# Kernel optimization log

Measured on AMD Instinct MI355X. Metric: run time of the kernel, lower is better.

The kernel has to match this reference:

```python
import jax, jax.numpy as jnp
import numpy as np

HEADS = 8
SPLITS = 4


def setup_inputs() -> dict:
    key = jax.random.key(0)
    ks = jax.random.split(key, 5)
    B, C, N = 8, 512, 4096
    C2 = C // 2
    x = jax.random.normal(ks[0], (B, C, N), jnp.float32)
    # reduction: Conv1d(C -> C//2, k=1) => weight [C2, C], bias [C2]
    Wr = jax.random.normal(ks[1], (C2, C), jnp.float32) * (1.0 / np.sqrt(C))
    br = jnp.zeros((C2,), jnp.float32)
    # toQKV: Linear(C2 -> 3*C2, bias=False); stored as [in, out]
    Wqkv = jax.random.normal(ks[2], (C2, 3 * C2), jnp.float32) * (1.0 / np.sqrt(C2))
    # expansion: Conv1d(C2 -> C, k=1) => weight [C, C2], bias [C]
    We = jax.random.normal(ks[3], (C, C2), jnp.float32) * (1.0 / np.sqrt(C2))
    be = jnp.zeros((C,), jnp.float32)
    return {"x": x, "Wr": Wr, "br": br, "Wqkv": Wqkv, "We": We, "be": be}


def reference(x, Wr, br, Wqkv, We, be):
    B, C, N = x.shape
    h, S = HEADS, SPLITS
    # 1x1 conv reduction: [B, C, N] -> [B, C2, N]
    y = jnp.einsum('oc,bcn->bon', Wr, x) + br[None, :, None]
    t = y.transpose(0, 2, 1)                       # [B, N, C2]
    qkv = t @ Wqkv                                 # [B, N, 3*C2]
    q, k, v = jnp.split(qkv, 3, axis=-1)
    d = q.shape[-1] // h
    n = N // S

    def to_chunks(a):
        # b n (h d) -> b h S n' d  (block-diagonal chunks along the token dim)
        return a.reshape(B, N, h, d).transpose(0, 2, 1, 3).reshape(B, h, S, n, d)

    q, k, v = to_chunks(q), to_chunks(k), to_chunks(v)
    scale = d ** -0.5
    scores = jnp.einsum('bhsnd,bhsmd->bhsnm', q, k) * scale   # [B,h,S,n,n]
    attn = jax.nn.softmax(scores, axis=-1)
    o = jnp.einsum('bhsnm,bhsmd->bhsnd', attn, v)             # [B,h,S,n,d]
    # rearrange per-chunk to 'b n (h d)' and concat chunks along n (restores order)
    o = o.transpose(0, 2, 3, 1, 4).reshape(B, N, h * d)       # [B, N, C2]
    o = o.transpose(0, 2, 1)                                  # [B, C2, N]
    out = jnp.einsum('oc,bcn->bon', We, o) + be[None, :, None]  # [B, C, N]
    return out
```

## Files before the change

kernel.cpp:

```cpp
#include <hip/hip_runtime.h>
#include <hip/hip_bf16.h>

#define BATCH 8
#define CIN   512
#define NTOK  4096
#define CH    256
#define J3    768
#define NH    8
#define DH    32
#define NCH   1024

typedef _Float16 F16;
typedef _Float16 f16x8 __attribute__((ext_vector_type(8)));
typedef _Float16 f16x4 __attribute__((ext_vector_type(4)));
typedef _Float16 f16x2 __attribute__((ext_vector_type(2)));
typedef float    f32x4  __attribute__((ext_vector_type(4)));
typedef float    f32x16 __attribute__((ext_vector_type(16)));

#define QSCALE 0.25503483f


__global__ __launch_bounds__(256) void fuse_weights_kernel(
    const float* __restrict__ Wr, const float* __restrict__ br,
    const float* __restrict__ Wqkv,
    F16* __restrict__ Wc_t, float* __restrict__ bcomb)
{
    const int j0 = blockIdx.x * 2;
    const int tid = threadIdx.x;
    float a00 = 0.f, a01 = 0.f, a10 = 0.f, a11 = 0.f;
    for (int c2 = 0; c2 < CH; ++c2) {
        const float w0 = Wr[c2 * CIN + tid];
        const float w1 = Wr[c2 * CIN + tid + 256];
        const float q0 = Wqkv[c2 * J3 + j0];
        const float q1 = Wqkv[c2 * J3 + j0 + 1];
        a00 = fmaf(w0, q0, a00);
        a01 = fmaf(w1, q0, a01);
        a10 = fmaf(w0, q1, a10);
        a11 = fmaf(w1, q1, a11);
    }
    const int c0 = tid, c1 = tid + 256;
    const int off0 = (c0 >> 5) * 8192 + ((c0 >> 3) & 3) * 2048 + (c0 & 7);
    const int off1 = (c1 >> 5) * 8192 + ((c1 >> 3) & 3) * 2048 + (c1 & 7);
#pragma unroll
    for (int jj = 0; jj < 2; ++jj) {
        const int j = j0 + jj;
        const float qs = (j < 256) ? QSCALE : 1.0f;
        const int jb = j >> 8, row = j & 255;
        const float v0 = jj ? a10 : a00, v1 = jj ? a11 : a01;
        Wc_t[jb * 131072 + off0 + row * 8] = (F16)(v0 * qs);
        Wc_t[jb * 131072 + off1 + row * 8] = (F16)(v1 * qs);
    }
    if (tid < 2) {
        const int j = j0 + tid;
        const float qs = (j < 256) ? QSCALE : 1.0f;
        float s = 0.f;
        for (int c2 = 0; c2 < CH; ++c2) s = fmaf(Wqkv[c2 * J3 + j], br[c2], s);
        bcomb[j] = s * qs;
    }
}

__global__ __launch_bounds__(256) void convert_we_kernel(
    const float* __restrict__ We, F16* __restrict__ We_t)
{
    const int i = blockIdx.x * 256 + threadIdx.x;
    const int j = i >> 8, c2 = i & 255;
    We_t[(j >> 7) * 32768 + (c2 >> 5) * 4096 + ((c2 >> 3) & 3) * 1024 +
         (j & 127) * 8 + (c2 & 7)] = (F16)We[i];
}

__global__ __launch_bounds__(256) void transpose_convert_kernel(
    const float* __restrict__ x, F16* __restrict__ xt_t)
{
    const int b = blockIdx.z;
    const int c0 = blockIdx.y * 8;
    const int n = blockIdx.x * 256 + threadIdx.x;

    const float* xb = x + ((size_t)b * CIN + c0) * NTOK + n;
    f16x8 v;
#pragma unroll
    for (int i = 0; i < 8; ++i)
        v[i] = (F16)xb[(size_t)i * NTOK];

    const int nb = n >> 7, row = n & 127;
    const int t = c0 >> 5, kg = (c0 >> 3) & 3;
    *(f16x8*)&xt_t[(size_t)b * 2097152 + nb * 65536 + t * 4096 + kg * 1024 +
                   row * 8] = v;
}

__global__ __launch_bounds__(512, 4) void gemm1_kernel(
    const F16* __restrict__ A,
    const F16* __restrict__ B,
    const float* __restrict__ bias,
    F16* __restrict__ Qb,
    F16* __restrict__ Kt,
    F16* __restrict__ Vt)
{
    const int b  = blockIdx.z;
    const int jb = blockIdx.y;
    const int j0 = jb * 256;
    const int nb = blockIdx.x;
    const int n0 = nb * 128;
    const int tid = threadIdx.x;
    const int w = tid >> 6, l = tid & 63;
    const int wr = w >> 1;
    const int wc = w & 1;
    const int cl = l & 15, rg = l >> 4;

    __shared__ __align__(16) char smem[49152];
    F16* Ash0 = (F16*)smem;
    F16* Ash1 = (F16*)(smem + 16384);
    F16* Bsh0 = (F16*)(smem + 32768);
    F16* Bsh1 = (F16*)(smem + 40960);
    F16* Esh  = (F16*)smem;

    f32x4 acc[4][4];
#pragma unroll
    for (int i = 0; i < 4; ++i)
#pragma unroll
        for (int j = 0; j < 4; ++j) acc[i][j] = (f32x4){0.f, 0.f, 0.f, 0.f};

    const F16* Abase = A + jb * 131072 + tid * 8;
    const F16* Bbase = B + (size_t)b * 2097152 + nb * 65536 + tid * 8;

#define G1_STAGE(Adst, Bdst, t)                                                \
    do {                                                                       \
        __builtin_amdgcn_global_load_lds(                                      \
            (const __attribute__((address_space(1))) void*)(Abase + (t) * 8192),\
            (__attribute__((address_space(3))) void*)&Adst[tid * 8], 16, 0, 0);\
        __builtin_amdgcn_global_load_lds(                                      \
            (const __attribute__((address_space(1))) void*)(Abase + (t) * 8192 \
                + 4096),                                                       \
            (__attribute__((address_space(3))) void*)&Adst[4096 + tid * 8],    \
            16, 0, 0);                                                         \
        __builtin_amdgcn_global_load_lds(                                      \
            (const __attribute__((address_space(1))) void*)(Bbase + (t) * 4096),\
            (__attribute__((address_space(3))) void*)&Bdst[tid * 8], 16, 0, 0);\
    } while (0)

    G1_STAGE(Ash0, Bsh0, 0);
    __syncthreads();

    for (int t = 0; t < 16; ++t) {
        F16* Ac = (t & 1) ? Ash1 : Ash0;
        F16* Bc = (t & 1) ? Bsh1 : Bsh0;
        if (t < 15) {
            F16* An = (t & 1) ? Ash0 : Ash1;
            F16* Bn = (t & 1) ? Bsh0 : Bsh1;
            G1_STAGE(An, Bn, t + 1);
        }
        f16x8 bf[4];
#pragma unroll
        for (int j = 0; j < 4; ++j)
            bf[j] = *(const f16x8*)&Bc[rg * 1024 + (wc * 64 + j * 16 + cl) * 8];
#pragma unroll
        for (int i = 0; i < 4; ++i) {
            const f16x8 af =
                *(const f16x8*)&Ac[rg * 2048 + (wr * 64 + i * 16 + cl) * 8];
#pragma unroll
            for (int j = 0; j < 4; ++j)
                acc[i][j] = __builtin_amdgcn_mfma_f32_16x16x32_f16(
                    af, bf[j], acc[i][j], 0, 0, 0);
        }
        __syncthreads();
    }
#undef G1_STAGE

    const int sidx = n0 >> 10;
    const int tb   = (n0 >> 6) & 15;

    if (jb < 2) {
        const size_t bN = (size_t)b * NTOK;
#pragma unroll
        for (int c = 0; c < 4; ++c) {
            if (c) __syncthreads();
            if (wc == (c >> 1)) {
#pragma unroll
                for (int i = 0; i < 4; ++i) {
#pragma unroll
                    for (int jj = 0; jj < 2; ++jj) {
                        const int jn = (c & 1) * 2 + jj;
                        const int nl = jj * 16 + cl;
                        const int jl = wr * 64 + i * 16 + rg * 4;
                        const int jg = j0 + jl;
                        f16x4 v;
#pragma unroll
                        for (int r = 0; r < 4; ++r)
                            v[r] = (F16)(acc[i][jn][r] + bias[jg + r]);
                        *(f16x4*)&Esh[nl * 264 + jl] = v;
                    }
                }
            }
            __syncthreads();
            if (jb == 0) {
                const int rr = tid >> 4, ss = tid & 15;
                const f16x8 ov0 = *(const f16x8*)&Esh[rr * 264 + ss * 16];
                const f16x8 ov1 = *(const f16x8*)&Esh[rr * 264 + ss * 16 + 8];
                F16* dst = &Qb[(bN + n0 + c * 32 + rr) * 256 + ss * 16];
                *(f16x8*)dst = ov0;
                *(f16x8*)(dst + 8) = ov1;
            } else {
                const int tloc = (tb + (c >> 1)) & 15;
#pragma unroll
                for (int p = 0; p < 2; ++p) {
                    const int uid = tid + p * 512;
                    const int nl = uid & 31, kg = (uid >> 5) & 3,
                              hh = uid >> 7;
                    const f16x8 ov =
                        *(const f16x8*)&Esh[nl * 264 + hh * 32 + kg * 8];
                    const int nk = (c & 1) * 32 + nl;
                    *(f16x8*)&Kt[(((size_t)b * NH + hh) * 4 + sidx) * 32768 +
                                 tloc * 2048 + kg * 512 + nk * 8] = ov;
                }
            }
        }
    } else {
#pragma unroll
        for (int c = 0; c < 4; ++c) {
            if (c) __syncthreads();
            if (wr == c) {
#pragma unroll
                for (int i = 0; i < 4; ++i) {
                    const int jg = j0 + c * 64 + i * 16 + rg * 4;
#pragma unroll
                    for (int jn = 0; jn < 4; ++jn) {
                        const int nl = wc * 64 + jn * 16 + cl;
#pragma unroll
                        for (int r = 0; r < 4; ++r)
                            Esh[(i * 16 + rg * 4 + r) * 136 + nl] =
                                (F16)(acc[i][jn][r] + bias[jg + r]);
                    }
                }
            }
            __syncthreads();
#pragma unroll
            for (int p = 0; p < 2; ++p) {
                const int uid = tid + p * 512;
                const int d = uid & 31, vg = (uid >> 5) & 7,
                          ttv = (uid >> 8) & 1, hl = uid >> 9;
                const int hh = c * 2 + hl;
                const int tloc = (tb + ttv) & 15;
                const f16x8 ov =
                    *(const f16x8*)&Esh[(hl * 32 + d) * 136 + ttv * 64 + vg * 8];
                *(f16x8*)&Vt[(((size_t)b * NH + hh) * 4 + sidx) * 32768 +
                             tloc * 2048 + vg * 256 + d * 8] = ov;
            }
        }
    }
}

__global__ __launch_bounds__(256, 4) void attn_mfma_kernel(
    const F16* __restrict__ Qb,
    const F16* __restrict__ Kt,
    const F16* __restrict__ Vt,
    F16* __restrict__ O)
{
    const int bid = blockIdx.x;
    const int xcd = bid & 7, tt = bid >> 3;
    const int qpair = tt & 3;
    const int pr = xcd * 32 + (tt >> 2);
    const int s = pr & 3, bh = pr >> 2;
    const int b = bh >> 3, h = bh & 7;
    const int tid = threadIdx.x;
    const int w = tid >> 6, l = tid & 63;
    const int ln = l & 31;
    const int hi = l >> 5;

    __shared__ __align__(16) F16 Klds[2][64 * 40];
    __shared__ __align__(16) F16 Vlds[2][32 * 68];

    const size_t bN = (size_t)b * NTOK + (size_t)s * NCH;
    const int q0 = qpair * 256 + w * 64;

    const F16* Qpa = Qb + (bN + q0 + ln) * 256 + h * DH + hi * 8;
    const F16* Qpb = Qpa + 32 * 256;
    const f16x8 qfa0 = *(const f16x8*)Qpa;
    const f16x8 qfa1 = *(const f16x8*)(Qpa + 16);
    const f16x8 qfb0 = *(const f16x8*)Qpb;
    const f16x8 qfb1 = *(const f16x8*)(Qpb + 16);

    const F16* Kbase = Kt + (((size_t)b * NH + h) * 4 + s) * 32768 + tid * 8;
    const F16* Vbase = Vt + (((size_t)b * NH + h) * 4 + s) * 32768 + tid * 8;
    const int kw = (tid & 63) * 40 + (tid >> 6) * 8;
    const int vw = (tid & 31) * 68 + (tid >> 5) * 8;

    f16x8 kreg = *(const f16x8*)Kbase;
    f16x8 vreg = *(const f16x8*)Vbase;

    f32x16 oacca = (f32x16)(0.0f);
    f32x16 oaccb = (f32x16)(0.0f);
    float lsum_a = 0.f, lsum_b = 0.f;

    *(f16x8*)&Klds[0][kw] = kreg;
    *(f16x4*)&Vlds[0][vw] = __builtin_shufflevector(vreg, vreg, 0, 1, 2, 3);
    *(f16x4*)&Vlds[0][vw + 4] = __builtin_shufflevector(vreg, vreg, 4, 5, 6, 7);

    for (int t = 0; t < 16; ++t) {
        const int cur = t & 1, nxt = cur ^ 1;
        __syncthreads();
        if (t < 15) {
            kreg = *(const f16x8*)(Kbase + (t + 1) * 2048);
            vreg = *(const f16x8*)(Vbase + (t + 1) * 2048);
        }
        const F16* Kb = &Klds[cur][0];
        const F16* Vb = &Vlds[cur][0];
#pragma unroll
        for (int u = 0; u < 2; ++u) {
            const int nkb = u * 32;
            const f16x8 kf0 = *(const f16x8*)&Kb[(nkb + ln) * 40 + hi * 8];
            const f16x8 kf1 = *(const f16x8*)&Kb[(nkb + ln) * 40 + 16 + hi * 8];

            f32x16 sacc = (f32x16)(0.0f);
            __builtin_amdgcn_s_setprio(1);
            sacc = __builtin_amdgcn_mfma_f32_32x32x16_f16(kf0, qfa0, sacc, 0, 0, 0);
            sacc = __builtin_amdgcn_mfma_f32_32x32x16_f16(kf1, qfa1, sacc, 0, 0, 0);
            __builtin_amdgcn_s_setprio(0);
            union { f16x8 v; f16x2 h[4]; } pa0, pa1, pb0, pb1;
#pragma unroll
            for (int e = 0; e < 4; ++e) {
                pa0.h[e] = __builtin_bit_cast(f16x2, __builtin_amdgcn_cvt_pkrtz(
                    __builtin_amdgcn_exp2f(sacc[2 * e]),
                    __builtin_amdgcn_exp2f(sacc[2 * e + 1])));
                pa1.h[e] = __builtin_bit_cast(f16x2, __builtin_amdgcn_cvt_pkrtz(
                    __builtin_amdgcn_exp2f(sacc[8 + 2 * e]),
                    __builtin_amdgcn_exp2f(sacc[8 + 2 * e + 1])));
            }
            {
                const f16x2 t01 = pa0.h[0] + pa0.h[1] + pa1.h[0] + pa1.h[1];
                const f16x2 t23 = pa0.h[2] + pa0.h[3] + pa1.h[2] + pa1.h[3];
                const f16x2 ts = t01 + t23;
                lsum_a += (float)ts[0] + (float)ts[1];
            }

            f32x16 sb = (f32x16)(0.0f);
            __builtin_amdgcn_s_setprio(1);
            sb = __builtin_amdgcn_mfma_f32_32x32x16_f16(kf0, qfb0, sb, 0, 0, 0);
            sb = __builtin_amdgcn_mfma_f32_32x32x16_f16(kf1, qfb1, sb, 0, 0, 0);
            __builtin_amdgcn_s_setprio(0);
#pragma unroll
            for (int e = 0; e < 4; ++e) {
                pb0.h[e] = __builtin_bit_cast(f16x2, __builtin_amdgcn_cvt_pkrtz(
                    __builtin_amdgcn_exp2f(sb[2 * e]),
                    __builtin_amdgcn_exp2f(sb[2 * e + 1])));
                pb1.h[e] = __builtin_bit_cast(f16x2, __builtin_amdgcn_cvt_pkrtz(
                    __builtin_amdgcn_exp2f(sb[8 + 2 * e]),
                    __builtin_amdgcn_exp2f(sb[8 + 2 * e + 1])));
            }
            {
                const f16x2 t01 = pb0.h[0] + pb0.h[1] + pb1.h[0] + pb1.h[1];
                const f16x2 t23 = pb0.h[2] + pb0.h[3] + pb1.h[2] + pb1.h[3];
                const f16x2 ts = t01 + t23;
                lsum_b += (float)ts[0] + (float)ts[1];
            }

            const int vbase = ln * 68 + nkb + 4 * hi;
            const f16x4 v00 = *(const f16x4*)&Vb[vbase];
            const f16x4 v01 = *(const f16x4*)&Vb[vbase + 8];
            const f16x4 v10 = *(const f16x4*)&Vb[vbase + 16];
            const f16x4 v11 = *(const f16x4*)&Vb[vbase + 24];
            const f16x8 vf0 = __builtin_shufflevector(v00, v01, 0, 1, 2, 3, 4, 5, 6, 7);
            const f16x8 vf1 = __builtin_shufflevector(v10, v11, 0, 1, 2, 3, 4, 5, 6, 7);

            __builtin_amdgcn_s_setprio(1);
            oacca = __builtin_amdgcn_mfma_f32_32x32x16_f16(pa0.v, vf0, oacca, 0, 0, 0);
            oacca = __builtin_amdgcn_mfma_f32_32x32x16_f16(pa1.v, vf1, oacca, 0, 0, 0);
            oaccb = __builtin_amdgcn_mfma_f32_32x32x16_f16(pb0.v, vf0, oaccb, 0, 0, 0);
            oaccb = __builtin_amdgcn_mfma_f32_32x32x16_f16(pb1.v, vf1, oaccb, 0, 0, 0);
            __builtin_amdgcn_s_setprio(0);
        }
        if (t < 15) {
            *(f16x8*)&Klds[nxt][kw] = kreg;
            *(f16x4*)&Vlds[nxt][vw] =
                __builtin_shufflevector(vreg, vreg, 0, 1, 2, 3);
            *(f16x4*)&Vlds[nxt][vw + 4] =
                __builtin_shufflevector(vreg, vreg, 4, 5, 6, 7);
        }
    }

    lsum_a += __shfl_xor(lsum_a, 32);
    lsum_b += __shfl_xor(lsum_b, 32);
    __syncthreads();
    float* Ltab = (float*)&Vlds[0][0] + w * 64;
    if (hi == 0) {
        Ltab[ln] = lsum_a;
        Ltab[32 + ln] = lsum_b;
    }
    F16* Elds = (F16*)&Klds[0][0] + w * 1152;
    const int q = ln;
#pragma unroll
    for (int set = 0; set < 2; ++set) {
        const f32x16 oacc = set ? oaccb : oacca;
#pragma unroll
        for (int r = 0; r < 16; ++r) {
            const int qr = (r & 3) + 8 * (r >> 2) + 4 * hi;
            const float invr = __builtin_amdgcn_rcpf(Ltab[set * 32 + qr]);
            Elds[qr * 36 + ln] = (F16)(oacc[r] * invr);
        }
        const int g = qpair * 256 + w * 64 + set * 32;
        const int nb = s * 8 + (g >> 7);
        const int row0 = g & 127;
        F16* Ob = O + (size_t)b * 1048576 + nb * 32768 + h * 4096;
#pragma unroll
        for (int st = 0; st < 2; ++st) {
            const int kg = hi + 2 * st;
            const f16x8 ov = *(const f16x8*)&Elds[q * 36 + kg * 8];
            *(f16x8*)&Ob[kg * 1024 + (row0 + q) * 8] = ov;
        }
    }
}

__global__ __launch_bounds__(256) void gemm2_kernel(
    const F16* __restrict__ A,
    const F16* __restrict__ B,
    const float* __restrict__ bias,
    float* __restrict__ Y)
{
    const int b  = blockIdx.z;
    const int jb = blockIdx.y;
    const int j0 = jb * 128;
    const int nb = blockIdx.x;
    const int n0 = nb * 128;
    const int tid = threadIdx.x;
    const int w = tid >> 6, l = tid & 63;
    const int wr = w >> 1, wc = w & 1;
    const int cl = l & 15, rg = l >> 4;

    __shared__ __align__(16) F16 Ash[2][4096];
    __shared__ __align__(16) F16 Bsh[2][4096];

    f32x4 acc[4][4];
#pragma unroll
    for (int i = 0; i < 4; ++i)
#pragma unroll
        for (int j = 0; j < 4; ++j) acc[i][j] = (f32x4){0.f, 0.f, 0.f, 0.f};

    const int frag_off = rg * 1024 + cl * 8;
    const F16* Abase = A + jb * 32768 + tid * 8;
    const F16* Bbase = B + (size_t)b * 1048576 + nb * 32768 + tid * 8;

#define G2_STAGE(bu, t)                                                        \
    do {                                                                       \
        __builtin_amdgcn_global_load_lds(                                      \
            (const __attribute__((address_space(1))) void*)(Abase + (t) * 4096),\
            (__attribute__((address_space(3))) void*)&Ash[bu][tid * 8],        \
            16, 0, 0);                                                         \
        __builtin_amdgcn_global_load_lds(                                      \
            (const __attribute__((address_space(1))) void*)(Abase + (t) * 4096 \
                + 2048),                                                       \
            (__attribute__((address_space(3))) void*)&Ash[bu][2048 + tid * 8], \
            16, 0, 0);                                                         \
        __builtin_amdgcn_global_load_lds(                                      \
            (const __attribute__((address_space(1))) void*)(Bbase + (t) * 4096),\
            (__attribute__((address_space(3))) void*)&Bsh[bu][tid * 8],        \
            16, 0, 0);                                                         \
        __builtin_amdgcn_global_load_lds(                                      \
            (const __attribute__((address_space(1))) void*)(Bbase + (t) * 4096 \
                + 2048),                                                       \
            (__attribute__((address_space(3))) void*)&Bsh[bu][2048 + tid * 8], \
            16, 0, 0);                                                         \
    } while (0)

    G2_STAGE(0, 0);
    __syncthreads();

    for (int t = 0; t < 8; ++t) {
        const int cur = t & 1;
        if (t < 7) G2_STAGE(cur ^ 1, t + 1);

        f16x8 af[4], bfr[4];
#pragma unroll
        for (int f = 0; f < 4; ++f) {
            af[f]  = *(const f16x8*)&Ash[cur][frag_off + (wr * 64 + f * 16) * 8];
            bfr[f] = *(const f16x8*)&Bsh[cur][frag_off + (wc * 64 + f * 16) * 8];
        }
#pragma unroll
        for (int i = 0; i < 4; ++i)
#pragma unroll
            for (int j = 0; j < 4; ++j)
                acc[i][j] = __builtin_amdgcn_mfma_f32_16x16x32_f16(
                    af[i], bfr[j], acc[i][j], 0, 0, 0);
        __syncthreads();
    }
#undef G2_STAGE

#pragma unroll
    for (int i = 0; i < 4; ++i) {
        const int jj = j0 + wr * 64 + i * 16 + rg * 4;
#pragma unroll
        for (int j = 0; j < 4; ++j) {
            const int nn = n0 + wc * 64 + j * 16 + cl;
#pragma unroll
            for (int r = 0; r < 4; ++r)
                Y[((size_t)b * CIN + jj + r) * NTOK + nn] =
                    acc[i][j][r] + bias[jj + r];
        }
    }
}

extern "C" void kernel_launch(void* const* d_in, const int* in_sizes, int n_in,
                              void* d_out, int out_size, void* d_ws, size_t ws_size,
                              hipStream_t stream)
{
    const float* x    = (const float*)d_in[0];
    const float* Wr   = (const float*)d_in[1];
    const float* br   = (const float*)d_in[2];
    const float* Wqkv = (const float*)d_in[3];
    const float* We   = (const float*)d_in[4];
    const float* be   = (const float*)d_in[5];
    float* out = (float*)d_out;

    char* ws = (char*)d_ws;
    F16*   Wc    = (F16*)ws;      ws += 786432;
    float* bcomb = (float*)ws;    ws += 4096;
    F16*   We_t  = (F16*)ws;      ws += 262144;
    F16*   Qb    = (F16*)ws;      ws += (size_t)BATCH * NTOK * 256 * 2;
    F16*   Kt    = (F16*)ws;      ws += (size_t)BATCH * NH * 4 * 32768 * 2;
    F16*   Vt    = (F16*)ws;      ws += (size_t)BATCH * NH * 4 * 32768 * 2;
    F16*   xt    = (F16*)ws;
    F16*   O_t   = (F16*)ws;

    fuse_weights_kernel<<<J3 / 2, 256, 0, stream>>>(Wr, br, Wqkv, Wc, bcomb);
    convert_we_kernel<<<CIN * CH / 256, 256, 0, stream>>>(We, We_t);
    transpose_convert_kernel<<<dim3(NTOK / 256, CIN / 8, BATCH), 256, 0, stream>>>(x, xt);
    gemm1_kernel<<<dim3(NTOK / 128, J3 / 256, BATCH), 512, 0, stream>>>(
        Wc, xt, bcomb, Qb, Kt, Vt);
    attn_mfma_kernel<<<1024, 256, 0, stream>>>(Qb, Kt, Vt, O_t);
    gemm2_kernel<<<dim3(NTOK / 128, CIN / 128, BATCH), 256, 0, stream>>>(
        We_t, O_t, be, out);
}
```

Measured before the change: 154.7 us.

## Load K/V fragments directly from global memory, drop LDS staging and barriers

Result: slower. 354.8 us (+129.4%).

```diff
diff --git a/kernel.cpp b/kernel.cpp
--- a/kernel.cpp
+++ b/kernel.cpp
@@ -248,7 +248,7 @@
     }
 }
 
-__global__ __launch_bounds__(256, 4) void attn_mfma_kernel(
+__global__ __launch_bounds__(256, 8) void attn_mfma_kernel(
     const F16* __restrict__ Qb,
     const F16* __restrict__ Kt,
     const F16* __restrict__ Vt,
@@ -265,8 +265,8 @@
     const int ln = l & 31;
     const int hi = l >> 5;
 
-    __shared__ __align__(16) F16 Klds[2][64 * 40];
-    __shared__ __align__(16) F16 Vlds[2][32 * 68];
+    __shared__ __align__(16) F16 Epi[4][1152];
+    __shared__ __align__(16) float Ltab_s[4][64];
 
     const size_t bN = (size_t)b * NTOK + (size_t)s * NCH;
     const int q0 = qpair * 256 + w * 64;
@@ -278,36 +278,20 @@
     const f16x8 qfb0 = *(const f16x8*)Qpb;
     const f16x8 qfb1 = *(const f16x8*)(Qpb + 16);
 
-    const F16* Kbase = Kt + (((size_t)b * NH + h) * 4 + s) * 32768 + tid * 8;
-    const F16* Vbase = Vt + (((size_t)b * NH + h) * 4 + s) * 32768 + tid * 8;
-    const int kw = (tid & 63) * 40 + (tid >> 6) * 8;
-    const int vw = (tid & 31) * 68 + (tid >> 5) * 8;
-
-    f16x8 kreg = *(const f16x8*)Kbase;
-    f16x8 vreg = *(const f16x8*)Vbase;
+    const F16* Kb = Kt + (((size_t)b * NH + h) * 4 + s) * 32768;
+    const F16* Vb = Vt + (((size_t)b * NH + h) * 4 + s) * 32768;
 
     f32x16 oacca = (f32x16)(0.0f);
     f32x16 oaccb = (f32x16)(0.0f);
     float lsum_a = 0.f, lsum_b = 0.f;
 
-    *(f16x8*)&Klds[0][kw] = kreg;
-    *(f16x4*)&Vlds[0][vw] = __builtin_shufflevector(vreg, vreg, 0, 1, 2, 3);
-    *(f16x4*)&Vlds[0][vw + 4] = __builtin_shufflevector(vreg, vreg, 4, 5, 6, 7);
-
     for (int t = 0; t < 16; ++t) {
-        const int cur = t & 1, nxt = cur ^ 1;
-        __syncthreads();
-        if (t < 15) {
-            kreg = *(const f16x8*)(Kbase + (t + 1) * 2048);
-            vreg = *(const f16x8*)(Vbase + (t + 1) * 2048);
-        }
-        const F16* Kb = &Klds[cur][0];
-        const F16* Vb = &Vlds[cur][0];
 #pragma unroll
         for (int u = 0; u < 2; ++u) {
-            const int nkb = u * 32;
-            const f16x8 kf0 = *(const f16x8*)&Kb[(nkb + ln) * 40 + hi * 8];
-            const f16x8 kf1 = *(const f16x8*)&Kb[(nkb + ln) * 40 + 16 + hi * 8];
+            const f16x8 kf0 =
+                *(const f16x8*)&Kb[t * 2048 + hi * 512 + (u * 32 + ln) * 8];
+            const f16x8 kf1 =
+                *(const f16x8*)&Kb[t * 2048 + (2 + hi) * 512 + (u * 32 + ln) * 8];
 
             f32x16 sacc = (f32x16)(0.0f);
             __builtin_amdgcn_s_setprio(1);
@@ -352,11 +336,11 @@
                 lsum_b += (float)ts[0] + (float)ts[1];
             }
 
-            const int vbase = ln * 68 + nkb + 4 * hi;
-            const f16x4 v00 = *(const f16x4*)&Vb[vbase];
-            const f16x4 v01 = *(const f16x4*)&Vb[vbase + 8];
-            const f16x4 v10 = *(const f16x4*)&Vb[vbase + 16];
-            const f16x4 v11 = *(const f16x4*)&Vb[vbase + 24];
+            const int vb0 = t * 2048 + (u * 4) * 256 + ln * 8 + 4 * hi;
+            const f16x4 v00 = *(const f16x4*)&Vb[vb0];
+            const f16x4 v01 = *(const f16x4*)&Vb[vb0 + 256];
+            const f16x4 v10 = *(const f16x4*)&Vb[vb0 + 512];
+            const f16x4 v11 = *(const f16x4*)&Vb[vb0 + 768];
             const f16x8 vf0 = __builtin_shufflevector(v00, v01, 0, 1, 2, 3, 4, 5, 6, 7);
             const f16x8 vf1 = __builtin_shufflevector(v10, v11, 0, 1, 2, 3, 4, 5, 6, 7);
 
@@ -367,24 +351,16 @@
             oaccb = __builtin_amdgcn_mfma_f32_32x32x16_f16(pb1.v, vf1, oaccb, 0, 0, 0);
             __builtin_amdgcn_s_setprio(0);
         }
-        if (t < 15) {
-            *(f16x8*)&Klds[nxt][kw] = kreg;
-            *(f16x4*)&Vlds[nxt][vw] =
-                __builtin_shufflevector(vreg, vreg, 0, 1, 2, 3);
-            *(f16x4*)&Vlds[nxt][vw + 4] =
-                __builtin_shufflevector(vreg, vreg, 4, 5, 6, 7);
-        }
     }
 
     lsum_a += __shfl_xor(lsum_a, 32);
     lsum_b += __shfl_xor(lsum_b, 32);
-    __syncthreads();
-    float* Ltab = (float*)&Vlds[0][0] + w * 64;
+    float* Ltab = &Ltab_s[w][0];
     if (hi == 0) {
         Ltab[ln] = lsum_a;
         Ltab[32 + ln] = lsum_b;
     }
-    F16* Elds = (F16*)&Klds[0][0] + w * 1152;
+    F16* Elds = &Epi[w][0];
     const int q = ln;
 #pragma unroll
     for (int set = 0; set < 2; ++set) {
```

## Enlarge gemm2 output tile to 256 rows with 512-thread blocks

Applied to the files above, without the earlier changes.

Result: no change. 153.6 us (-0.7%).

```diff
diff --git a/kernel.cpp b/kernel.cpp
--- a/kernel.cpp
+++ b/kernel.cpp
@@ -64,8 +64,8 @@
 {
     const int i = blockIdx.x * 256 + threadIdx.x;
     const int j = i >> 8, c2 = i & 255;
-    We_t[(j >> 7) * 32768 + (c2 >> 5) * 4096 + ((c2 >> 3) & 3) * 1024 +
-         (j & 127) * 8 + (c2 & 7)] = (F16)We[i];
+    We_t[(j >> 8) * 65536 + (c2 >> 5) * 8192 + ((c2 >> 3) & 3) * 2048 +
+         (j & 255) * 8 + (c2 & 7)] = (F16)We[i];
 }
 
 __global__ __launch_bounds__(256) void transpose_convert_kernel(
@@ -408,7 +408,7 @@
     }
 }
 
-__global__ __launch_bounds__(256) void gemm2_kernel(
+__global__ __launch_bounds__(512, 4) void gemm2_kernel(
     const F16* __restrict__ A,
     const F16* __restrict__ B,
     const float* __restrict__ bias,
@@ -416,16 +416,20 @@
 {
     const int b  = blockIdx.z;
     const int jb = blockIdx.y;
-    const int j0 = jb * 128;
+    const int j0 = jb * 256;
     const int nb = blockIdx.x;
     const int n0 = nb * 128;
     const int tid = threadIdx.x;
     const int w = tid >> 6, l = tid & 63;
-    const int wr = w >> 1, wc = w & 1;
+    const int wr = w >> 1;
+    const int wc = w & 1;
     const int cl = l & 15, rg = l >> 4;
 
-    __shared__ __align__(16) F16 Ash[2][4096];
-    __shared__ __align__(16) F16 Bsh[2][4096];
+    __shared__ __align__(16) char smem[49152];
+    F16* Ash0 = (F16*)smem;
+    F16* Ash1 = (F16*)(smem + 16384);
+    F16* Bsh0 = (F16*)(smem + 32768);
+    F16* Bsh1 = (F16*)(smem + 40960);
 
     f32x4 acc[4][4];
 #pragma unroll
@@ -433,51 +437,48 @@
 #pragma unroll
         for (int j = 0; j < 4; ++j) acc[i][j] = (f32x4){0.f, 0.f, 0.f, 0.f};
 
-    const int frag_off = rg * 1024 + cl * 8;
-    const F16* Abase = A + jb * 32768 + tid * 8;
+    const F16* Abase = A + jb * 65536 + tid * 8;
     const F16* Bbase = B + (size_t)b * 1048576 + nb * 32768 + tid * 8;
 
-#define G2_STAGE(bu, t)                                                        \
+#define G2_STAGE(Adst, Bdst, t)                                                \
     do {                                                                       \
         __builtin_amdgcn_global_load_lds(                                      \
-            (const __attribute__((address_space(1))) void*)(Abase + (t) * 4096),\
-            (__attribute__((address_space(3))) void*)&Ash[bu][tid * 8],        \
-            16, 0, 0);                                                         \
+            (const __attribute__((address_space(1))) void*)(Abase + (t) * 8192),\
+            (__attribute__((address_space(3))) void*)&Adst[tid * 8], 16, 0, 0);\
         __builtin_amdgcn_global_load_lds(                                      \
-            (const __attribute__((address_space(1))) void*)(Abase + (t) * 4096 \
-                + 2048),                                                       \
-            (__attribute__((address_space(3))) void*)&Ash[bu][2048 + tid * 8], \
+            (const __attribute__((address_space(1))) void*)(Abase + (t) * 8192 \
+                + 4096),                                                       \
+            (__attribute__((address_space(3))) void*)&Adst[4096 + tid * 8],    \
             16, 0, 0);                                                         \
         __builtin_amdgcn_global_load_lds(                                      \
             (const __attribute__((address_space(1))) void*)(Bbase + (t) * 4096),\
-            (__attribute__((address_space(3))) void*)&Bsh[bu][tid * 8],        \
-            16, 0, 0);                                                         \
-        __builtin_amdgcn_global_load_lds(                                      \
-            (const __attribute__((address_space(1))) void*)(Bbase + (t) * 4096 \
-                + 2048),                                                       \
-            (__attribute__((address_space(3))) void*)&Bsh[bu][2048 + tid * 8], \
-            16, 0, 0);                                                         \
+            (__attribute__((address_space(3))) void*)&Bdst[tid * 8], 16, 0, 0);\
     } while (0)
 
-    G2_STAGE(0, 0);
+    G2_STAGE(Ash0, Bsh0, 0);
     __syncthreads();
 
     for (int t = 0; t < 8; ++t) {
-        const int cur = t & 1;
-        if (t < 7) G2_STAGE(cur ^ 1, t + 1);
-
-        f16x8 af[4], bfr[4];
-#pragma unroll
-        for (int f = 0; f < 4; ++f) {
-            af[f]  = *(const f16x8*)&Ash[cur][frag_off + (wr * 64 + f * 16) * 8];
-            bfr[f] = *(const f16x8*)&Bsh[cur][frag_off + (wc * 64 + f * 16) * 8];
-        }
-#pragma unroll
-        for (int i = 0; i < 4; ++i)
+        F16* Ac = (t & 1) ? Ash1 : Ash0;
+        F16* Bc = (t & 1) ? Bsh1 : Bsh0;
+        if (t < 7) {
+            F16* An = (t & 1) ? Ash0 : Ash1;
+            F16* Bn = (t & 1) ? Bsh0 : Bsh1;
+            G2_STAGE(An, Bn, t + 1);
+        }
+        f16x8 bf[4];
+#pragma unroll
+        for (int j = 0; j < 4; ++j)
+            bf[j] = *(const f16x8*)&Bc[rg * 1024 + (wc * 64 + j * 16 + cl) * 8];
+#pragma unroll
+        for (int i = 0; i < 4; ++i) {
+            const f16x8 af =
+                *(const f16x8*)&Ac[rg * 2048 + (wr * 64 + i * 16 + cl) * 8];
 #pragma unroll
             for (int j = 0; j < 4; ++j)
                 acc[i][j] = __builtin_amdgcn_mfma_f32_16x16x32_f16(
-                    af[i], bfr[j], acc[i][j], 0, 0, 0);
+                    af, bf[j], acc[i][j], 0, 0, 0);
+        }
         __syncthreads();
     }
 #undef G2_STAGE
@@ -524,6 +525,6 @@
     gemm1_kernel<<<dim3(NTOK / 128, J3 / 256, BATCH), 512, 0, stream>>>(
         Wc, xt, bcomb, Qb, Kt, Vt);
     attn_mfma_kernel<<<1024, 256, 0, stream>>>(Qb, Kt, Vt, O_t);
-    gemm2_kernel<<<dim3(NTOK / 128, CIN / 128, BATCH), 256, 0, stream>>>(
+    gemm2_kernel<<<dim3(NTOK / 128, CIN / 256, BATCH), 512, 0, stream>>>(
         We_t, O_t, be, out);
 }
```
